# Kernel optimization log

Hardware: AMD Instinct MI355X
Metric: run time of the kernel (lower is better)

## Reference

```python
import jax, jax.numpy as jnp
import numpy as np

B, N, E, H = 4, 4096, 1024, 16
D = E // H


def setup_inputs() -> dict:
    key = jax.random.key(0)
    ks = jax.random.split(key, 8)
    s = 1.0 / np.sqrt(E)
    x = jax.random.normal(ks[0], (B, N, E), dtype=jnp.float32)
    # binary multiplicative sparsity pattern over the head-head score matrix
    sparsity_pattern = jax.random.randint(ks[1], (H, H), 0, 2).astype(jnp.float32)
    Wq = jax.random.normal(ks[2], (E, E), dtype=jnp.float32) * s
    bq = jax.random.normal(ks[3], (E,), dtype=jnp.float32) * s
    Wk = jax.random.normal(ks[4], (E, E), dtype=jnp.float32) * s
    bk = jax.random.normal(ks[5], (E,), dtype=jnp.float32) * s
    Wv = jax.random.normal(ks[6], (E, E), dtype=jnp.float32) * s
    bv = jax.random.normal(ks[7], (E,), dtype=jnp.float32) * s
    return {"x": x, "sparsity_pattern": sparsity_pattern,
            "Wq": Wq, "bq": bq, "Wk": Wk, "bk": bk, "Wv": Wv, "bv": bv}


def reference(x, sparsity_pattern, Wq, bq, Wk, bk, Wv, bv):
    b, n, e = x.shape
    # torch Linear: y = x @ W.T + b
    q = (x @ Wq.T + bq).reshape(b, n, H, D)
    k = (x @ Wk.T + bk).reshape(b, n, H, D)
    v = (x @ Wv.T + bv).reshape(b, n, H, D)
    # torch.matmul over last two dims of [B,N,H,D]: scores are [B,N,H,H]
    scores = jnp.einsum('bnhd,bngd->bnhg', q, k) * sparsity_pattern
    attn = jax.nn.softmax(scores, axis=-1)
    out = jnp.einsum('bnhg,bngd->bnhd', attn, v).reshape(b, n, e)
    return out
```

## Files before the change

kernel.cpp:

```cpp
#include <hip/hip_runtime.h>
#include <hip/hip_bf16.h>

#define M_   16384
#define K_   1024
#define NQKV 3072

typedef _Float16 f16x4 __attribute__((ext_vector_type(4)));
typedef _Float16 f16x8 __attribute__((ext_vector_type(8)));
typedef float    f32x4 __attribute__((ext_vector_type(4)));

__global__ __launch_bounds__(256) void cvt_f32_f16(const float* __restrict__ in,
                                                   _Float16* __restrict__ o, int n4) {
  int i = blockIdx.x * blockDim.x + threadIdx.x;
  const int stride = gridDim.x * blockDim.x;
  for (; i < n4; i += stride) {
    float4 v = ((const float4*)in)[i];
    f16x4 h; h[0] = (_Float16)v.x; h[1] = (_Float16)v.y;
    h[2] = (_Float16)v.z; h[3] = (_Float16)v.w;
    *(f16x4*)&o[(size_t)i * 4] = h;
  }
}

__global__ __launch_bounds__(256) void cvt3_f32_f16(
    const float* __restrict__ a, const float* __restrict__ b,
    const float* __restrict__ c, _Float16* __restrict__ o, int n4each) {
  const float* src = (blockIdx.y == 0) ? a : (blockIdx.y == 1) ? b : c;
  _Float16* dst = o + (size_t)blockIdx.y * n4each * 4;
  int i = blockIdx.x * blockDim.x + threadIdx.x;
  const int stride = gridDim.x * blockDim.x;
  for (; i < n4each; i += stride) {
    float4 v = ((const float4*)src)[i];
    f16x4 h; h[0] = (_Float16)v.x; h[1] = (_Float16)v.y;
    h[2] = (_Float16)v.z; h[3] = (_Float16)v.w;
    *(f16x4*)&dst[(size_t)i * 4] = h;
  }
}

__global__ __launch_bounds__(512, 2) void gemm_qkv(
    const _Float16* __restrict__ xh, const _Float16* __restrict__ wh,
    const float* __restrict__ bq, const float* __restrict__ bk,
    const float* __restrict__ bv, _Float16* __restrict__ qkv)
{
  __shared__ __align__(16) _Float16 As[2][256 * 64];
  __shared__ __align__(16) _Float16 Bs[2][256 * 64];

  const int tid  = threadIdx.x;
  const int ln   = tid & 63;
  const int w    = tid >> 6;
  const int wm2  = w >> 2;
  const int wn4  = w & 3;
  const int lcol = ln & 15, quad = ln >> 4;

  const int bid = blockIdx.x;
  const int swz = (bid & 7) * 96 + (bid >> 3);
  const int m0 = (swz / 12) * 256;
  const int n0 = (swz % 12) * 256;

  f32x4 acc[8][4];
#pragma unroll
  for (int i = 0; i < 8; ++i)
#pragma unroll
    for (int j = 0; j < 4; ++j) acc[i][j] = f32x4{0.f, 0.f, 0.f, 0.f};

  f16x8 a[4][2], b[2][2];

#define STAGE_A(BUF, KT, X)                                                    \
  { _Pragma("unroll")                                                          \
    for (int j = 0; j < 2; ++j) {                                              \
      const int c   = j * 512 + tid;                                           \
      const int rr  = c >> 3;                                                  \
      const int r   = (X) * 64 + (rr & 63) + ((rr >> 6) << 7);                 \
      const int cb  = (c & 7) ^ (r & 7);                                       \
      const int rr0 = j * 64 + w * 8;                                          \
      const int r0  = (X) * 64 + (rr0 & 63) + ((rr0 >> 6) << 7);               \
      __builtin_amdgcn_global_load_lds(                                        \
          (const __attribute__((address_space(1))) void*)(                     \
              xh + (size_t)(m0 + r) * K_ + (KT) * 64 + cb * 8),                \
          (__attribute__((address_space(3))) void*)(&As[BUF][r0 * 64]),        \
          16, 0, 0);                                                           \
    } }

#define STAGE_B(BUF, KT, Y)                                                    \
  { _Pragma("unroll")                                                          \
    for (int j = 0; j < 2; ++j) {                                              \
      const int c   = j * 512 + tid;                                           \
      const int rr  = c >> 3;                                                  \
      const int r   = ((rr >> 5) << 6) + (Y) * 32 + (rr & 31);                 \
      const int cb  = (c & 7) ^ (r & 7);                                       \
      const int rr0 = j * 64 + w * 8;                                          \
      const int r0  = ((rr0 >> 5) << 6) + (Y) * 32 + (rr0 & 31);               \
      __builtin_amdgcn_global_load_lds(                                        \
          (const __attribute__((address_space(1))) void*)(                     \
              wh + (size_t)(n0 + r) * K_ + (KT) * 64 + cb * 8),                \
          (__attribute__((address_space(3))) void*)(&Bs[BUF][r0 * 64]),        \
          16, 0, 0);                                                           \
    } }

#define LOADA(BUF, MH)                                                         \
  _Pragma("unroll")                                                            \
  for (int mi = 0; mi < 4; ++mi) {                                             \
    const int ar = wm2 * 128 + (MH) * 64 + mi * 16 + lcol;                     \
    const int sw = ar & 7;                                                     \
    a[mi][0] = *(const f16x8*)&As[BUF][ar * 64 + ((quad    ) ^ sw) * 8];       \
    a[mi][1] = *(const f16x8*)&As[BUF][ar * 64 + ((quad + 4) ^ sw) * 8];       \
  }

#define LOADB(BUF, NH)                                                         \
  _Pragma("unroll")                                                            \
  for (int ni = 0; ni < 2; ++ni) {                                             \
    const int br = wn4 * 64 + (NH) * 32 + ni * 16 + lcol;                      \
    const int sw = br & 7;                                                     \
    b[ni][0] = *(const f16x8*)&Bs[BUF][br * 64 + ((quad    ) ^ sw) * 8];       \
    b[ni][1] = *(const f16x8*)&Bs[BUF][br * 64 + ((quad + 4) ^ sw) * 8];       \
  }

#define MFMA16(MH, NH)                                                         \
  __builtin_amdgcn_s_setprio(1);                                               \
  _Pragma("unroll")                                                            \
  for (int kb = 0; kb < 2; ++kb)                                               \
    _Pragma("unroll")                                                          \
    for (int mi = 0; mi < 4; ++mi)                                             \
      _Pragma("unroll")                                                        \
      for (int ni = 0; ni < 2; ++ni)                                           \
        acc[(MH) * 4 + mi][(NH) * 2 + ni] =                                    \
            __builtin_amdgcn_mfma_f32_16x16x32_f16(                            \
                a[mi][kb], b[ni][kb], acc[(MH) * 4 + mi][(NH) * 2 + ni],       \
                0, 0, 0);                                                      \
  __builtin_amdgcn_s_setprio(0);

#define BAR()  { __builtin_amdgcn_s_barrier(); __builtin_amdgcn_sched_barrier(0); }
#define LGKM0() { asm volatile("s_waitcnt lgkmcnt(0)" ::: "memory");           \
                  __builtin_amdgcn_sched_barrier(0); }
#define VM6() asm volatile("s_waitcnt vmcnt(6)" ::: "memory")
#define VM0() asm volatile("s_waitcnt vmcnt(0)" ::: "memory")

#define GITER(KT0, LAST)                                                       \
  {                                                                   \
    LOADA(0, 0); LOADB(0, 0); STAGE_A(1, (KT0) + 1, 0);                        \
    BAR(); LGKM0(); MFMA16(0, 0); BAR();                                       \
                                                                      \
    LOADA(0, 1); if (!(LAST)) STAGE_B(0, (KT0) + 2, 0);                        \
    BAR(); LGKM0(); MFMA16(1, 0); BAR();                                       \
                                                                      \
    LOADB(0, 1); if (!(LAST)) STAGE_A(0, (KT0) + 2, 1);                        \
    BAR(); LGKM0(); MFMA16(1, 1); BAR();                                       \
                                                                      \
    LOADA(0, 0); if (!(LAST)) STAGE_B(0, (KT0) + 2, 1);                        \
    if (LAST) { VM0(); } else { VM6(); }                                       \
    BAR(); LGKM0(); MFMA16(0, 1); BAR();                                       \
                                                                      \
    LOADA(1, 0); LOADB(1, 0); if (!(LAST)) STAGE_A(0, (KT0) + 2, 0);           \
    BAR(); LGKM0(); MFMA16(0, 0); BAR();                                       \
                                                                      \
    LOADA(1, 1); if (!(LAST)) STAGE_B(1, (KT0) + 3, 0);                        \
    BAR(); LGKM0(); MFMA16(1, 0); BAR();                                       \
                                                                      \
    LOADB(1, 1); if (!(LAST)) STAGE_A(1, (KT0) + 3, 1);                        \
    BAR(); LGKM0(); MFMA16(1, 1); BAR();                                       \
                                                                      \
    LOADA(1, 0); if (!(LAST)) { STAGE_B(1, (KT0) + 3, 1); VM6(); }             \
    BAR(); LGKM0(); MFMA16(0, 1); BAR();                                       \
  }

  STAGE_A(0, 0, 0); STAGE_B(0, 0, 0); STAGE_A(0, 0, 1); STAGE_B(0, 0, 1);
  STAGE_B(1, 1, 0); STAGE_A(1, 1, 1); STAGE_B(1, 1, 1);
  VM6(); BAR();

#pragma unroll 1
  for (int it = 0; it < 7; ++it) { GITER(it * 2, 0); }
  GITER(14, 1);

#pragma unroll
  for (int nh = 0; nh < 4; ++nh) {
    const int col = n0 + wn4 * 64 + nh * 16 + lcol;
    const int seg = col >> 10, cs = col & 1023;
    const float bi = ((seg == 0) ? bq : (seg == 1) ? bk : bv)[cs];
#pragma unroll
    for (int mi = 0; mi < 8; ++mi) {
      const int r0 = m0 + wm2 * 128 + mi * 16 + quad * 4;
#pragma unroll
      for (int r = 0; r < 4; ++r)
        qkv[(size_t)(r0 + r) * 3072 + col] = (_Float16)(acc[mi][nh][r] + bi);
    }
  }
#undef STAGE_A
#undef STAGE_B
#undef LOADA
#undef LOADB
#undef MFMA16
#undef BAR
#undef LGKM0
#undef VM6
#undef VM0
#undef GITER
}

__global__ __launch_bounds__(256) void attn_kernel(
    const _Float16* __restrict__ qkv,
    const float* __restrict__ pat,
    float* __restrict__ out)
{
  __shared__ float pat_s[256];
  __shared__ __align__(16) _Float16 Ps[4][16 * 24];
  __shared__ __align__(16) _Float16 Vt[4][64 * 24];

  const int tid  = threadIdx.x;
  const int ln   = tid & 63;
  const int wv   = tid >> 6;
  const int lcol = ln & 15, quad = ln >> 4;
  const int t    = blockIdx.x * 4 + wv;

  pat_s[tid] = pat[tid];
  __syncthreads();

  const _Float16* qg = qkv + (size_t)t * 3072;
  const _Float16* kg = qg + 1024;
  const _Float16* vg = qg + 2048;

#pragma unroll
  for (int i = 0; i < 2; i++) {
    const int e = i * 64 + ln;
    const int g = e >> 3, c = (e & 7) * 8;
    f16x8 vc = *(const f16x8*)(vg + g * 64 + c);
#pragma unroll
    for (int j = 0; j < 8; j++) Vt[wv][(c + j) * 24 + g] = vc[j];
  }

  f16x8 aq0 = *(const f16x8*)(qg + lcol * 64 + quad * 8);
  f16x8 aq1 = *(const f16x8*)(qg + lcol * 64 + 32 + quad * 8);
  f16x8 bk0 = *(const f16x8*)(kg + lcol * 64 + quad * 8);
  f16x8 bk1 = *(const f16x8*)(kg + lcol * 64 + 32 + quad * 8);
  f32x4 s = {0.f, 0.f, 0.f, 0.f};
  s = __builtin_amdgcn_mfma_f32_16x16x32_f16(aq0, bk0, s, 0, 0, 0);
  s = __builtin_amdgcn_mfma_f32_16x16x32_f16(aq1, bk1, s, 0, 0, 0);

#pragma unroll
  for (int r = 0; r < 4; r++) {
    const float sv = s[r] * pat_s[(quad * 4 + r) * 16 + lcol];
    float m = sv;
#pragma unroll
    for (int msk = 1; msk < 16; msk <<= 1) m = fmaxf(m, __shfl_xor(m, msk, 64));
    const float e = __expf(sv - m);
    float su = e;
#pragma unroll
    for (int msk = 1; msk < 16; msk <<= 1) su += __shfl_xor(su, msk, 64);
    Ps[wv][(quad * 4 + r) * 24 + lcol] = (_Float16)(e / su);
  }

  f16x8 ap = {};
  if (quad < 2) ap = *(const f16x8*)&Ps[wv][lcol * 24 + quad * 8];

  f32x4 o[4];
#pragma unroll
  for (int dt = 0; dt < 4; dt++) {
    f16x8 bvf = {};
    if (quad < 2) bvf = *(const f16x8*)&Vt[wv][(dt * 16 + lcol) * 24 + quad * 8];
    f32x4 z = {0.f, 0.f, 0.f, 0.f};
    o[dt] = __builtin_amdgcn_mfma_f32_16x16x32_f16(ap, bvf, z, 0, 0, 0);
  }

  float* op = out + (size_t)t * 1024;
#pragma unroll
  for (int dt = 0; dt < 4; dt++)
#pragma unroll
    for (int r = 0; r < 4; r++)
      op[(quad * 4 + r) * 64 + dt * 16 + lcol] = o[dt][r];
}

extern "C" void kernel_launch(void* const* d_in, const int* in_sizes, int n_in,
                              void* d_out, int out_size, void* d_ws, size_t ws_size,
                              hipStream_t stream) {
  const float* x   = (const float*)d_in[0];
  const float* pat = (const float*)d_in[1];
  const float* Wq  = (const float*)d_in[2];
  const float* bq  = (const float*)d_in[3];
  const float* Wk  = (const float*)d_in[4];
  const float* bk  = (const float*)d_in[5];
  const float* Wv  = (const float*)d_in[6];
  const float* bv  = (const float*)d_in[7];

  _Float16* qkvh = (_Float16*)d_ws;
  _Float16* xh   = qkvh + (size_t)50331648;
  _Float16* wh   = qkvh + (size_t)67108864;

  cvt_f32_f16<<<4096, 256, 0, stream>>>(x, xh, 4194304);
  cvt3_f32_f16<<<dim3(256, 3), 256, 0, stream>>>(Wq, Wk, Wv, wh, 262144);

  gemm_qkv<<<768, 512, 0, stream>>>(xh, wh, bq, bk, bv, qkvh);
  attn_kernel<<<M_ / 4, 256, 0, stream>>>(qkvh, pat, (float*)d_out);
}
```

Baseline: 283.5 us.

## Split GEMM LDS reads per k-half with partial lgkm waits; streamline attention

The QKV GEMM main loop now double-buffers its register fragments (a0/a1, b0/b1) and splits each LDS fragment read into two k-halves. It waits with partial lgkmcnt counts so the first half's MFMAs can start while the second half's reads are still in flight, and it reuses the A fragments across sub-tiles instead of reloading them. The attention kernel drops the shared-memory pattern copy and its __syncthreads, reading the pattern straight into registers. It also issues the V loads together with the Q/K loads and replaces the zero-padded 16x16x32 MFMA with a 16x16x16 MFMA for the P·V product. The cost is higher register pressure and a more fragile manual wait-count schedule.

```diff
diff --git a/kernel.cpp b/kernel.cpp
--- a/kernel.cpp
+++ b/kernel.cpp
@@ -62,7 +62,7 @@
 #pragma unroll
     for (int j = 0; j < 4; ++j) acc[i][j] = f32x4{0.f, 0.f, 0.f, 0.f};
 
-  f16x8 a[4][2], b[2][2];
+  f16x8 a0[4][2], a1[4][2], b0[2][2], b1[2][2];
 
 #define STAGE_A(BUF, KT, X)                                                    \
   { _Pragma("unroll")                                                          \
@@ -96,70 +96,61 @@
           16, 0, 0);                                                           \
     } }
 
-#define LOADA(BUF, MH)                                                         \
+#define RDA(DST, BUF, MH, KB)                                                  \
   _Pragma("unroll")                                                            \
   for (int mi = 0; mi < 4; ++mi) {                                             \
     const int ar = wm2 * 128 + (MH) * 64 + mi * 16 + lcol;                     \
     const int sw = ar & 7;                                                     \
-    a[mi][0] = *(const f16x8*)&As[BUF][ar * 64 + ((quad    ) ^ sw) * 8];       \
-    a[mi][1] = *(const f16x8*)&As[BUF][ar * 64 + ((quad + 4) ^ sw) * 8];       \
-  }
-
-#define LOADB(BUF, NH)                                                         \
+    DST[mi][KB] = *(const f16x8*)&As[BUF][ar * 64 + (((KB)*4 + quad) ^ sw) * 8]; \
+  }
+
+#define RDB(DST, BUF, NH, KB)                                                  \
   _Pragma("unroll")                                                            \
   for (int ni = 0; ni < 2; ++ni) {                                             \
     const int br = wn4 * 64 + (NH) * 32 + ni * 16 + lcol;                      \
     const int sw = br & 7;                                                     \
-    b[ni][0] = *(const f16x8*)&Bs[BUF][br * 64 + ((quad    ) ^ sw) * 8];       \
-    b[ni][1] = *(const f16x8*)&Bs[BUF][br * 64 + ((quad + 4) ^ sw) * 8];       \
-  }
-
-#define MFMA16(MH, NH)                                                         \
+    DST[ni][KB] = *(const f16x8*)&Bs[BUF][br * 64 + (((KB)*4 + quad) ^ sw) * 8]; \
+  }
+
+#define MFMA8(AARR, BARR, MH, NH, KB)                                          \
   __builtin_amdgcn_s_setprio(1);                                               \
   _Pragma("unroll")                                                            \
-  for (int kb = 0; kb < 2; ++kb)                                               \
+  for (int mi = 0; mi < 4; ++mi)                                               \
     _Pragma("unroll")                                                          \
-    for (int mi = 0; mi < 4; ++mi)                                             \
-      _Pragma("unroll")                                                        \
-      for (int ni = 0; ni < 2; ++ni)                                           \
-        acc[(MH) * 4 + mi][(NH) * 2 + ni] =                                    \
-            __builtin_amdgcn_mfma_f32_16x16x32_f16(                            \
-                a[mi][kb], b[ni][kb], acc[(MH) * 4 + mi][(NH) * 2 + ni],       \
-                0, 0, 0);                                                      \
+    for (int ni = 0; ni < 2; ++ni)                                             \
+      acc[(MH) * 4 + mi][(NH) * 2 + ni] =                                      \
+          __builtin_amdgcn_mfma_f32_16x16x32_f16(                              \
+              AARR[mi][KB], BARR[ni][KB], acc[(MH) * 4 + mi][(NH) * 2 + ni],   \
+              0, 0, 0);                                                        \
   __builtin_amdgcn_s_setprio(0);
 
-#define BAR()  { __builtin_amdgcn_s_barrier(); __builtin_amdgcn_sched_barrier(0); }
-#define LGKM0() { asm volatile("s_waitcnt lgkmcnt(0)" ::: "memory");           \
-                  __builtin_amdgcn_sched_barrier(0); }
-#define VM6() asm volatile("s_waitcnt vmcnt(6)" ::: "memory")
-#define VM0() asm volatile("s_waitcnt vmcnt(0)" ::: "memory")
-
-#define GITER(KT0, LAST)                                                       \
-  {                                                                   \
-    LOADA(0, 0); LOADB(0, 0); STAGE_A(1, (KT0) + 1, 0);                        \
-    BAR(); LGKM0(); MFMA16(0, 0); BAR();                                       \
-                                                                      \
-    LOADA(0, 1); if (!(LAST)) STAGE_B(0, (KT0) + 2, 0);                        \
-    BAR(); LGKM0(); MFMA16(1, 0); BAR();                                       \
-                                                                      \
-    LOADB(0, 1); if (!(LAST)) STAGE_A(0, (KT0) + 2, 1);                        \
-    BAR(); LGKM0(); MFMA16(1, 1); BAR();                                       \
-                                                                      \
-    LOADA(0, 0); if (!(LAST)) STAGE_B(0, (KT0) + 2, 1);                        \
-    if (LAST) { VM0(); } else { VM6(); }                                       \
-    BAR(); LGKM0(); MFMA16(0, 1); BAR();                                       \
-                                                                      \
-    LOADA(1, 0); LOADB(1, 0); if (!(LAST)) STAGE_A(0, (KT0) + 2, 0);           \
-    BAR(); LGKM0(); MFMA16(0, 0); BAR();                                       \
-                                                                      \
-    LOADA(1, 1); if (!(LAST)) STAGE_B(1, (KT0) + 3, 0);                        \
-    BAR(); LGKM0(); MFMA16(1, 0); BAR();                                       \
-                                                                      \
-    LOADB(1, 1); if (!(LAST)) STAGE_A(1, (KT0) + 3, 1);                        \
-    BAR(); LGKM0(); MFMA16(1, 1); BAR();                                       \
-                                                                      \
-    LOADA(1, 0); if (!(LAST)) { STAGE_B(1, (KT0) + 3, 1); VM6(); }             \
-    BAR(); LGKM0(); MFMA16(0, 1); BAR();                                       \
+#define SB()    __builtin_amdgcn_sched_barrier(0)
+#define BAR()   { __builtin_amdgcn_s_barrier(); SB(); }
+#define LGKM(N) { asm volatile("s_waitcnt lgkmcnt(" #N ")" ::: "memory"); SB(); }
+#define VM6()   asm volatile("s_waitcnt vmcnt(6)" ::: "memory")
+#define VM0()   asm volatile("s_waitcnt vmcnt(0)" ::: "memory")
+
+#define KTILE(BUF, STG1, STG2, STG3, STG4, WAIT4)                              \
+  {                                               \
+    RDB(b0, BUF, 0, 0); RDA(a0, BUF, 0, 0); SB();                              \
+    RDB(b0, BUF, 0, 1); RDA(a0, BUF, 0, 1); SB();                              \
+    STG1;                                                                      \
+    BAR(); LGKM(6);  MFMA8(a0, b0, 0, 0, 0);                                   \
+           LGKM(0);  MFMA8(a0, b0, 0, 0, 1); BAR();                            \
+                                                        \
+    RDA(a1, BUF, 1, 0); SB(); RDA(a1, BUF, 1, 1); SB();                        \
+    STG2;                                                                      \
+    BAR(); LGKM(4);  MFMA8(a1, b0, 1, 0, 0);                                   \
+           LGKM(0);  MFMA8(a1, b0, 1, 0, 1); BAR();                            \
+                                                        \
+    RDB(b1, BUF, 1, 0); SB(); RDB(b1, BUF, 1, 1); SB();                        \
+    STG3;                                                                      \
+    BAR(); LGKM(2);  MFMA8(a1, b1, 1, 1, 0);                                   \
+           LGKM(0);  MFMA8(a1, b1, 1, 1, 1); BAR();                            \
+                                                 \
+    STG4; WAIT4;                                                               \
+    BAR();           MFMA8(a0, b1, 0, 1, 0);                                   \
+                     MFMA8(a0, b1, 0, 1, 1); BAR();                            \
   }
 
   STAGE_A(0, 0, 0); STAGE_B(0, 0, 0); STAGE_A(0, 0, 1); STAGE_B(0, 0, 1);
@@ -167,8 +158,15 @@
   VM6(); BAR();
 
 #pragma unroll 1
-  for (int it = 0; it < 7; ++it) { GITER(it * 2, 0); }
-  GITER(14, 1);
+  for (int it = 0; it < 7; ++it) {
+    const int kt = it * 2;
+    KTILE(0, STAGE_A(1, kt + 1, 0), STAGE_B(0, kt + 2, 0),
+             STAGE_A(0, kt + 2, 1), STAGE_B(0, kt + 2, 1), VM6());
+    KTILE(1, STAGE_A(0, kt + 2, 0), STAGE_B(1, kt + 3, 0),
+             STAGE_A(1, kt + 3, 1), STAGE_B(1, kt + 3, 1), VM6());
+  }
+  KTILE(0, STAGE_A(1, 15, 0), , , , VM0());
+  KTILE(1, , , , , );
 
 #pragma unroll
   for (int nh = 0; nh < 4; ++nh) {
@@ -185,14 +183,15 @@
   }
 #undef STAGE_A
 #undef STAGE_B
-#undef LOADA
-#undef LOADB
-#undef MFMA16
+#undef RDA
+#undef RDB
+#undef MFMA8
+#undef SB
 #undef BAR
-#undef LGKM0
+#undef LGKM
 #undef VM6
 #undef VM0
-#undef GITER
+#undef KTILE
 }
 
 __global__ __launch_bounds__(256) void attn_kernel(
@@ -200,7 +199,6 @@
     const float* __restrict__ pat,
     float* __restrict__ out)
 {
-  __shared__ float pat_s[256];
   __shared__ __align__(16) _Float16 Ps[4][16 * 24];
   __shared__ __align__(16) _Float16 Vt[4][64 * 24];
 
@@ -210,33 +208,35 @@
   const int lcol = ln & 15, quad = ln >> 4;
   const int t    = blockIdx.x * 4 + wv;
 
-  pat_s[tid] = pat[tid];
-  __syncthreads();
-
   const _Float16* qg = qkv + (size_t)t * 3072;
   const _Float16* kg = qg + 1024;
   const _Float16* vg = qg + 2048;
 
-#pragma unroll
-  for (int i = 0; i < 2; i++) {
-    const int e = i * 64 + ln;
-    const int g = e >> 3, c = (e & 7) * 8;
-    f16x8 vc = *(const f16x8*)(vg + g * 64 + c);
-#pragma unroll
-    for (int j = 0; j < 8; j++) Vt[wv][(c + j) * 24 + g] = vc[j];
-  }
-
+  f16x8 vc[2];
+  vc[0] = *(const f16x8*)(vg + ((ln >> 3)    ) * 64 + (ln & 7) * 8);
+  vc[1] = *(const f16x8*)(vg + ((ln >> 3) + 8) * 64 + (ln & 7) * 8);
   f16x8 aq0 = *(const f16x8*)(qg + lcol * 64 + quad * 8);
   f16x8 aq1 = *(const f16x8*)(qg + lcol * 64 + 32 + quad * 8);
   f16x8 bk0 = *(const f16x8*)(kg + lcol * 64 + quad * 8);
   f16x8 bk1 = *(const f16x8*)(kg + lcol * 64 + 32 + quad * 8);
+  float p4[4];
+#pragma unroll
+  for (int r = 0; r < 4; r++) p4[r] = pat[(quad * 4 + r) * 16 + lcol];
+
+#pragma unroll
+  for (int i = 0; i < 2; i++) {
+    const int g = (ln >> 3) + i * 8, c = (ln & 7) * 8;
+#pragma unroll
+    for (int j = 0; j < 8; j++) Vt[wv][(c + j) * 24 + g] = vc[i][j];
+  }
+
   f32x4 s = {0.f, 0.f, 0.f, 0.f};
   s = __builtin_amdgcn_mfma_f32_16x16x32_f16(aq0, bk0, s, 0, 0, 0);
   s = __builtin_amdgcn_mfma_f32_16x16x32_f16(aq1, bk1, s, 0, 0, 0);
 
 #pragma unroll
   for (int r = 0; r < 4; r++) {
-    const float sv = s[r] * pat_s[(quad * 4 + r) * 16 + lcol];
+    const float sv = s[r] * p4[r];
     float m = sv;
 #pragma unroll
     for (int msk = 1; msk < 16; msk <<= 1) m = fmaxf(m, __shfl_xor(m, msk, 64));
@@ -247,16 +247,14 @@
     Ps[wv][(quad * 4 + r) * 24 + lcol] = (_Float16)(e / su);
   }
 
-  f16x8 ap = {};
-  if (quad < 2) ap = *(const f16x8*)&Ps[wv][lcol * 24 + quad * 8];
+  f16x4 ap = *(const f16x4*)&Ps[wv][lcol * 24 + quad * 4];
 
   f32x4 o[4];
 #pragma unroll
   for (int dt = 0; dt < 4; dt++) {
-    f16x8 bvf = {};
-    if (quad < 2) bvf = *(const f16x8*)&Vt[wv][(dt * 16 + lcol) * 24 + quad * 8];
+    f16x4 bvf = *(const f16x4*)&Vt[wv][(dt * 16 + lcol) * 24 + quad * 4];
     f32x4 z = {0.f, 0.f, 0.f, 0.f};
-    o[dt] = __builtin_amdgcn_mfma_f32_16x16x32_f16(ap, bvf, z, 0, 0, 0);
+    o[dt] = __builtin_amdgcn_mfma_f32_16x16x16f16(ap, bvf, z, 0, 0, 0);
   }
 
   float* op = out + (size_t)t * 1024;
```

New measurement: 271.9 us. 1.04x faster.
